# Performance work log

Measured on AMD Instinct MI355X. Metric: run time of the kernel, lower is better.

## Reference

```python
import jax, jax.numpy as jnp
import numpy as np

N_NODES = 100000
N_EDGES = 1600000
N_GRAPHS = 1000
HID = 64
NEG_SLOPE = 0.2


def _glorot(key, shape):
    fan_in, fan_out = shape[0], shape[-1]
    lim = float(np.sqrt(6.0 / (fan_in + fan_out)))
    return jax.random.uniform(key, shape, jnp.float32, -lim, lim)


def setup_inputs() -> dict:
    key = jax.random.key(0)
    ks = jax.random.split(key, 20)
    x = jax.random.normal(ks[0], (N_NODES, 1), jnp.float32)
    edge_index = jax.random.randint(ks[1], (2, N_EDGES), 0, N_NODES, jnp.int64)
    batch = jnp.sort(jax.random.randint(ks[2], (N_NODES,), 0, N_GRAPHS, jnp.int64))
    inp = {"x": x, "edge_index": edge_index, "batch": batch}
    # GATv2Conv layer 1 (in=3 -> out=HID, 1 head)
    inp["Wl1"] = _glorot(ks[3], (3, HID)); inp["bl1"] = jnp.zeros((HID,), jnp.float32)
    inp["Wr1"] = _glorot(ks[4], (3, HID)); inp["br1"] = jnp.zeros((HID,), jnp.float32)
    inp["a1"] = _glorot(ks[5], (HID, 1))[:, 0]; inp["b1"] = jnp.zeros((HID,), jnp.float32)
    # GATv2Conv layer 2 (HID -> HID)
    inp["Wl2"] = _glorot(ks[6], (HID, HID)); inp["bl2"] = jnp.zeros((HID,), jnp.float32)
    inp["Wr2"] = _glorot(ks[7], (HID, HID)); inp["br2"] = jnp.zeros((HID,), jnp.float32)
    inp["a2"] = _glorot(ks[8], (HID, 1))[:, 0]; inp["b2"] = jnp.zeros((HID,), jnp.float32)
    # lin2 (HID -> 2)
    inp["W3"] = _glorot(ks[9], (HID, 2)); inp["b3"] = jnp.zeros((2,), jnp.float32)
    return inp


def gatv2_layer(x, src, dst, Wl, bl, Wr, br, a, b):
    """GATv2Conv, 1 head, add_self_loops=True, negative_slope=0.2."""
    n = x.shape[0]
    xl = x @ Wl + bl  # source-side transform [N, C]
    xr = x @ Wr + br  # target-side transform [N, C]
    loops = jnp.arange(n, dtype=src.dtype)
    s = jnp.concatenate([src, loops])
    d = jnp.concatenate([dst, loops])
    # per-edge attention logit: a^T LeakyReLU(xl[j] + xr[i])
    e = jax.nn.leaky_relu(xl[s] + xr[d], NEG_SLOPE) @ a  # [E+N]
    # segment softmax over incoming edges of each dst node
    m = jax.ops.segment_max(e, d, num_segments=n)
    ex = jnp.exp(e - m[d])
    denom = jax.ops.segment_sum(ex, d, num_segments=n)
    alpha = ex / denom[d]
    out = jax.ops.segment_sum(alpha[:, None] * xl[s], d, num_segments=n)
    return out + b


def reference(x, edge_index, batch, Wl1, bl1, Wr1, br1, a1, b1,
              Wl2, bl2, Wr2, br2, a2, b2, W3, b3):
    n = x.shape[0]
    src, dst = edge_index[0], edge_index[1]
    ones = jnp.ones((src.shape[0],), jnp.float32)
    deg_in = jax.ops.segment_sum(ones, dst, num_segments=n)   # bincount(dst)
    deg_out = jax.ops.segment_sum(ones, src, num_segments=n)  # bincount(src)
    h = jnp.concatenate([x, deg_in[:, None], deg_out[:, None]], axis=1)  # [N,3]
    h = gatv2_layer(h, src, dst, Wl1, bl1, Wr1, br1, a1, b1)
    h = jnp.tanh(h)
    h = gatv2_layer(h, src, dst, Wl2, bl2, Wr2, br2, a2, b2)
    # global_max_pool over graphs
    g = jax.ops.segment_max(h, batch, num_segments=N_GRAPHS)  # [G, HID]
    return g @ W3 + b3  # [G, 2]
```

## Files before the change

kernel.cpp:

```cpp
#include <hip/hip_runtime.h>
#include <hip/hip_bf16.h>
#include <hip/hip_fp16.h>

#define HID 64
#define NEG_SLOPE 0.2f
#define BLK_E 8192
#define EDGE_CAP 6144
#define NDB 16

typedef _Float16 f16x2 __attribute__((ext_vector_type(2)));


__global__ void k_hist2(const int* __restrict__ src, const int* __restrict__ dst,
                        int* __restrict__ histS, int* __restrict__ histD,
                        int E, int NB, int NBLK) {
    __shared__ int hs[512], hd[512];
    int t = threadIdx.x, blk = blockIdx.x;
    for (int b = t; b < NB; b += 1024) { hs[b] = 0; hd[b] = 0; }
    __syncthreads();
    int base = blk * BLK_E;
    #pragma unroll
    for (int k = 0; k < BLK_E / 1024; ++k) {
        int i = base + k * 1024 + t;
        if (i < E) {
            atomicAdd(&hs[src[i] >> 8], 1);
            atomicAdd(&hd[dst[i] >> 8], 1);
        }
    }
    __syncthreads();
    for (int b = t; b < NB; b += 1024) {
        histS[b * NBLK + blk] = hs[b];
        histD[b * NBLK + blk] = hd[b];
    }
}

__global__ void k_binscan(int* __restrict__ histS, int* __restrict__ histD,
                          int* __restrict__ totS, int* __restrict__ totD,
                          int NB, int NBLK) {
    __shared__ int s[256];
    int b = blockIdx.x;
    int* hist = histS; int* tot = totS;
    if (b >= NB) { b -= NB; hist = histD; tot = totD; }
    int t = threadIdx.x;
    int v = (t < NBLK) ? hist[b * NBLK + t] : 0;
    s[t] = v;
    __syncthreads();
    for (int o = 1; o < 256; o <<= 1) {
        int u = (t >= o) ? s[t - o] : 0;
        __syncthreads();
        s[t] += u;
        __syncthreads();
    }
    if (t < NBLK) hist[b * NBLK + t] = s[t] - v;
    if (t == 255) tot[b] = s[255];
}

__global__ void k_binoffset(const int* __restrict__ totS, const int* __restrict__ totD,
                            int* __restrict__ bsS, int* __restrict__ bsD,
                            int NB, int E, int* __restrict__ row_off, int N) {
    __shared__ int s[512];
    int t = threadIdx.x;
    int v = (t < NB) ? totS[t] : 0;
    s[t] = v; __syncthreads();
    for (int o = 1; o < 512; o <<= 1) {
        int u = (t >= o) ? s[t - o] : 0;
        __syncthreads(); s[t] += u; __syncthreads();
    }
    if (t < NB) bsS[t] = s[t] - v;
    if (t == 0) bsS[NB] = E;
    __syncthreads();
    v = (t < NB) ? totD[t] : 0;
    s[t] = v; __syncthreads();
    for (int o = 1; o < 512; o <<= 1) {
        int u = (t >= o) ? s[t - o] : 0;
        __syncthreads(); s[t] += u; __syncthreads();
    }
    if (t < NB) bsD[t] = s[t] - v;
    if (t == 0) { bsD[NB] = E; row_off[N] = E; }
}

__global__ void k_scatter_bins(const int* __restrict__ src, const int* __restrict__ dst,
                               const int* __restrict__ histS, const int* __restrict__ histD,
                               const int* __restrict__ bsS, const int* __restrict__ bsD,
                               unsigned* __restrict__ packS, unsigned* __restrict__ packD,
                               int E, int NB, int NBLK) {
    __shared__ int baseS[512], baseD[512];
    int t = threadIdx.x, blk = blockIdx.x;
    for (int b = t; b < NB; b += 1024) {
        baseS[b] = bsS[b] + histS[b * NBLK + blk];
        baseD[b] = bsD[b] + histD[b * NBLK + blk];
    }
    __syncthreads();
    int base = blk * BLK_E;
    #pragma unroll
    for (int k = 0; k < BLK_E / 1024; ++k) {
        int i = base + k * 1024 + t;
        if (i < E) {
            int sv = src[i], dv = dst[i];
            int pD = atomicAdd(&baseD[dv >> 8], 1);
            packD[pD] = ((unsigned)(dv & 255) << 24) | (unsigned)sv;
            int pS = atomicAdd(&baseS[sv >> 8], 1);
            packS[pS] = (unsigned)(sv & 255);
        }
    }
}

__global__ void k_csr_bin(const unsigned* __restrict__ packD, const int* __restrict__ bsD,
                          int* __restrict__ row_off, float* __restrict__ deg_in,
                          int* __restrict__ csr_src, int N) {
    __shared__ int cnt[256], off[256], cur[256];
    __shared__ unsigned eb[EDGE_CAP];
    int b = blockIdx.x, t = threadIdx.x;
    int lo = bsD[b], hi = bsD[b + 1], ne = hi - lo;
    bool fits = (ne <= EDGE_CAP);
    if (t < 256) cnt[t] = 0;
    __syncthreads();
    for (int i = t; i < ne; i += 1024) {
        unsigned v = packD[lo + i];
        if (fits) eb[i] = v;
        atomicAdd(&cnt[v >> 24], 1);
    }
    __syncthreads();
    if (t < 256) off[t] = cnt[t];
    __syncthreads();
    for (int o = 1; o < 256; o <<= 1) {
        int u = 0;
        if (t < 256 && t >= o) u = off[t - o];
        __syncthreads();
        if (t < 256) off[t] += u;
        __syncthreads();
    }
    if (t < 256) {
        int ex = off[t] - cnt[t];
        cur[t] = lo + ex;
        int node = b * 256 + t;
        if (node < N) {
            row_off[node] = lo + ex;
            deg_in[node] = (float)cnt[t];
        }
    }
    __syncthreads();
    for (int i = t; i < ne; i += 1024) {
        unsigned v = fits ? eb[i] : packD[lo + i];
        int pos = atomicAdd(&cur[v >> 24], 1);
        csr_src[pos] = (int)(v & 0xFFFFFFu);
    }
}

__global__ void k_cnt_bin(const unsigned* __restrict__ packS, const int* __restrict__ bsS,
                          float* __restrict__ deg_out, int N) {
    __shared__ int cnt[256];
    int b = blockIdx.x, t = threadIdx.x;
    int lo = bsS[b], hi = bsS[b + 1];
    if (t < 256) cnt[t] = 0;
    __syncthreads();
    for (int i = lo + t; i < hi; i += 1024) atomicAdd(&cnt[packS[i] & 255], 1);
    __syncthreads();
    if (t < 256) {
        int node = b * 256 + t;
        if (node < N) deg_out[node] = (float)cnt[t];
    }
}


__global__ void k_deghist(const float* __restrict__ deg_in, int* __restrict__ dhist, int N) {
    __shared__ int h[64];
    int t = threadIdx.x, b = blockIdx.x;
    if (t < 64) h[t] = 0;
    __syncthreads();
    int chunk = (N + NDB - 1) / NDB;
    int lo = b * chunk, hi = lo + chunk; if (hi > N) hi = N;
    for (int i = lo + t; i < hi; i += 1024) {
        int dg = (int)deg_in[i]; if (dg > 63) dg = 63;
        atomicAdd(&h[dg], 1);
    }
    __syncthreads();
    if (t < 64) dhist[t * NDB + b] = h[t];
}

__global__ void k_degscan(int* __restrict__ dhist) {
    __shared__ int s[1024];
    int t = threadIdx.x;
    int v = dhist[t];
    s[t] = v; __syncthreads();
    for (int o = 1; o < 1024; o <<= 1) {
        int u = (t >= o) ? s[t - o] : 0;
        __syncthreads(); s[t] += u; __syncthreads();
    }
    dhist[t] = s[t] - v;
}

__global__ void k_degscatter(const float* __restrict__ deg_in, const int* __restrict__ dhist,
                             int* __restrict__ perm, int N) {
    __shared__ int cur[64];
    int t = threadIdx.x, b = blockIdx.x;
    if (t < 64) cur[t] = dhist[t * NDB + b];
    __syncthreads();
    int chunk = (N + NDB - 1) / NDB;
    int lo = b * chunk, hi = lo + chunk; if (hi > N) hi = N;
    for (int i = lo + t; i < hi; i += 1024) {
        int dg = (int)deg_in[i]; if (dg > 63) dg = 63;
        int p = atomicAdd(&cur[dg], 1);
        perm[p] = i;
    }
}


__global__ void k_xfrm1(const float* __restrict__ x, const float* __restrict__ deg_in,
                        const float* __restrict__ deg_out,
                        const float* __restrict__ Wl, const float* __restrict__ bl,
                        const float* __restrict__ Wr, const float* __restrict__ br,
                        __half* __restrict__ A, __half* __restrict__ B, int N) {
    int idx = blockIdx.x * blockDim.x + threadIdx.x;
    if (idx >= N * HID) return;
    int n = idx >> 6, c = idx & 63;
    float h0 = x[n], h1 = deg_in[n], h2 = deg_out[n];
    A[idx] = __float2half(h0 * Wl[c] + h1 * Wl[HID + c] + h2 * Wl[2 * HID + c] + bl[c]);
    B[idx] = __float2half(h0 * Wr[c] + h1 * Wr[HID + c] + h2 * Wr[2 * HID + c] + br[c]);
}

struct H8 { f16x2 h[8]; };

__device__ __forceinline__ f16x2 bch2(unsigned u) {
    return __builtin_bit_cast(f16x2, u);
}

__device__ __forceinline__ H8 ldrow(const uint4* __restrict__ T, size_t base) {
    uint4 r0 = T[base], r1 = T[base + 1];
    H8 o;
    o.h[0] = bch2(r0.x); o.h[1] = bch2(r0.y); o.h[2] = bch2(r0.z); o.h[3] = bch2(r0.w);
    o.h[4] = bch2(r1.x); o.h[5] = bch2(r1.y); o.h[6] = bch2(r1.z); o.h[7] = bch2(r1.w);
    return o;
}

__device__ __forceinline__ float logit16(const H8& a, const H8& x,
                                         const float* __restrict__ awf, f16x2 ns2) {
    float t = 0.0f;
    #pragma unroll
    for (int j = 0; j < 8; ++j) {
        f16x2 s = a.h[j] + x.h[j];
        f16x2 l = __builtin_elementwise_max(s, ns2 * s);
        t = fmaf((float)l.x, awf[2 * j], t);
        t = fmaf((float)l.y, awf[2 * j + 1], t);
    }
    return t;
}

__device__ __forceinline__ void accum16(float* __restrict__ acc, const H8& a, float w) {
    #pragma unroll
    for (int j = 0; j < 8; ++j) {
        acc[2 * j]     = fmaf((float)a.h[j].x, w, acc[2 * j]);
        acc[2 * j + 1] = fmaf((float)a.h[j].y, w, acc[2 * j + 1]);
    }
}

template <bool TANH>
__global__ void k_gat_fused(const int* __restrict__ csr_src, const int* __restrict__ row_off,
                            const int* __restrict__ perm,
                            const __half* __restrict__ Ah, const __half* __restrict__ Bh,
                            const float* __restrict__ aw, const float* __restrict__ bias,
                            float* __restrict__ out, int N) {
    int tid = blockIdx.x * blockDim.x + threadIdx.x;
    int r = tid >> 2;
    int gl = threadIdx.x & 3;
    if (r >= N) return;
    int d = perm[N - 1 - r];

    const uint4* A16 = (const uint4*)Ah;
    const uint4* B16 = (const uint4*)Bh;
    f16x2 ns2;
    ns2.x = (_Float16)NEG_SLOPE; ns2.y = (_Float16)NEG_SLOPE;

    float awf[16];
    {
        const float4* a4 = (const float4*)aw;
        #pragma unroll
        for (int j = 0; j < 4; ++j) {
            float4 v = a4[gl * 4 + j];
            awf[4 * j] = v.x; awf[4 * j + 1] = v.y; awf[4 * j + 2] = v.z; awf[4 * j + 3] = v.w;
        }
    }

    size_t rowbase = (size_t)d * 8 + gl * 2;
    H8 xh = ldrow(B16, rowbase);
    H8 as = ldrow(A16, rowbase);

    float t = logit16(as, xh, awf, ns2);
    t += __shfl_xor(t, 1); t += __shfl_xor(t, 2);
    float m = t, denom = 1.0f;
    float acc[16];
    #pragma unroll
    for (int j = 0; j < 8; ++j) {
        acc[2 * j] = (float)as.h[j].x;
        acc[2 * j + 1] = (float)as.h[j].y;
    }

    int lo = row_off[d], hi = row_off[d + 1];
    int k = lo;
    for (; k + 3 < hi; k += 4) {
        int s0 = csr_src[k], s1 = csr_src[k + 1], s2 = csr_src[k + 2], s3 = csr_src[k + 3];
        H8 a0 = ldrow(A16, (size_t)s0 * 8 + gl * 2);
        H8 a1 = ldrow(A16, (size_t)s1 * 8 + gl * 2);
        H8 a2 = ldrow(A16, (size_t)s2 * 8 + gl * 2);
        H8 a3 = ldrow(A16, (size_t)s3 * 8 + gl * 2);
        float t0 = logit16(a0, xh, awf, ns2);
        float t1 = logit16(a1, xh, awf, ns2);
        float t2 = logit16(a2, xh, awf, ns2);
        float t3 = logit16(a3, xh, awf, ns2);
        t0 += __shfl_xor(t0, 1); t1 += __shfl_xor(t1, 1);
        t2 += __shfl_xor(t2, 1); t3 += __shfl_xor(t3, 1);
        t0 += __shfl_xor(t0, 2); t1 += __shfl_xor(t1, 2);
        t2 += __shfl_xor(t2, 2); t3 += __shfl_xor(t3, 2);
        float mx = fmaxf(fmaxf(t0, t1), fmaxf(t2, t3));
        if (mx > m) {
            float sc = __expf(m - mx);
            denom *= sc;
            #pragma unroll
            for (int j = 0; j < 16; ++j) acc[j] *= sc;
            m = mx;
        }
        float w0 = __expf(t0 - m), w1 = __expf(t1 - m);
        float w2 = __expf(t2 - m), w3 = __expf(t3 - m);
        denom += (w0 + w1) + (w2 + w3);
        accum16(acc, a0, w0);
        accum16(acc, a1, w1);
        accum16(acc, a2, w2);
        accum16(acc, a3, w3);
    }
    for (; k < hi; ++k) {
        int s0 = csr_src[k];
        H8 a0 = ldrow(A16, (size_t)s0 * 8 + gl * 2);
        float t0 = logit16(a0, xh, awf, ns2);
        t0 += __shfl_xor(t0, 1); t0 += __shfl_xor(t0, 2);
        if (t0 > m) {
            float sc = __expf(m - t0);
            denom *= sc;
            #pragma unroll
            for (int j = 0; j < 16; ++j) acc[j] *= sc;
            m = t0;
        }
        float w0 = __expf(t0 - m);
        denom += w0;
        accum16(acc, a0, w0);
    }

    float inv = 1.0f / denom;
    const float4* b4 = (const float4*)bias;
    float4* o4 = (float4*)out;
    #pragma unroll
    for (int j = 0; j < 4; ++j) {
        float4 bv = b4[gl * 4 + j];
        float4 o;
        o.x = acc[4 * j] * inv + bv.x;
        o.y = acc[4 * j + 1] * inv + bv.y;
        o.z = acc[4 * j + 2] * inv + bv.z;
        o.w = acc[4 * j + 3] * inv + bv.w;
        if (TANH) { o.x = tanhf(o.x); o.y = tanhf(o.y); o.z = tanhf(o.z); o.w = tanhf(o.w); }
        o4[(size_t)d * 16 + gl * 4 + j] = o;
    }
}

__global__ __launch_bounds__(512) void k_xfrm2(
        const float* __restrict__ H,
        const float* __restrict__ Wl, const float* __restrict__ bl,
        const float* __restrict__ Wr, const float* __restrict__ br,
        __half* __restrict__ A, __half* __restrict__ B, int N) {
    __shared__ float wls[4096];
    __shared__ float wrs[4096];
    __shared__ float hst[64 * 66];
    int t = threadIdx.x;
    int base = blockIdx.x * 64;

    ((float4*)wls)[t * 2]     = ((const float4*)Wl)[t * 2];
    ((float4*)wls)[t * 2 + 1] = ((const float4*)Wl)[t * 2 + 1];
    ((float4*)wrs)[t * 2]     = ((const float4*)Wr)[t * 2];
    ((float4*)wrs)[t * 2 + 1] = ((const float4*)Wr)[t * 2 + 1];

    #pragma unroll
    for (int u = 0; u < 2; ++u) {
        int j = t * 2 + u;
        int nd = j >> 4, c4 = j & 15;
        int node = base + nd;
        float4 hv = (node < N) ? ((const float4*)H)[(size_t)node * 16 + c4]
                               : make_float4(0.f, 0.f, 0.f, 0.f);
        hst[(c4 * 4 + 0) * 66 + nd] = hv.x;
        hst[(c4 * 4 + 1) * 66 + nd] = hv.y;
        hst[(c4 * 4 + 2) * 66 + nd] = hv.z;
        hst[(c4 * 4 + 3) * 66 + nd] = hv.w;
    }
    __syncthreads();

    int w = t >> 6, l = t & 63;
    float acL[8] = {0, 0, 0, 0, 0, 0, 0, 0};
    float acR[8] = {0, 0, 0, 0, 0, 0, 0, 0};
    #pragma unroll 4
    for (int kk = 0; kk < 64; ++kk) {
        float hv = hst[kk * 66 + l];
        const float4* wl4 = (const float4*)&wls[kk * 64 + w * 8];
        const float4* wr4 = (const float4*)&wrs[kk * 64 + w * 8];
        float4 w0 = wl4[0], w1 = wl4[1];
        float4 r0 = wr4[0], r1 = wr4[1];
        acL[0] = fmaf(hv, w0.x, acL[0]); acL[1] = fmaf(hv, w0.y, acL[1]);
        acL[2] = fmaf(hv, w0.z, acL[2]); acL[3] = fmaf(hv, w0.w, acL[3]);
        acL[4] = fmaf(hv, w1.x, acL[4]); acL[5] = fmaf(hv, w1.y, acL[5]);
        acL[6] = fmaf(hv, w1.z, acL[6]); acL[7] = fmaf(hv, w1.w, acL[7]);
        acR[0] = fmaf(hv, r0.x, acR[0]); acR[1] = fmaf(hv, r0.y, acR[1]);
        acR[2] = fmaf(hv, r0.z, acR[2]); acR[3] = fmaf(hv, r0.w, acR[3]);
        acR[4] = fmaf(hv, r1.x, acR[4]); acR[5] = fmaf(hv, r1.y, acR[5]);
        acR[6] = fmaf(hv, r1.z, acR[6]); acR[7] = fmaf(hv, r1.w, acR[7]);
    }

    int node = base + l;
    if (node < N) {
        float4 bl0 = ((const float4*)bl)[w * 2], bl1 = ((const float4*)bl)[w * 2 + 1];
        float4 br0 = ((const float4*)br)[w * 2], br1 = ((const float4*)br)[w * 2 + 1];
        __half2* A2 = (__half2*)A;
        __half2* B2 = (__half2*)B;
        size_t bo = (size_t)node * 32 + w * 4;
        A2[bo + 0] = __floats2half2_rn(acL[0] + bl0.x, acL[1] + bl0.y);
        A2[bo + 1] = __floats2half2_rn(acL[2] + bl0.z, acL[3] + bl0.w);
        A2[bo + 2] = __floats2half2_rn(acL[4] + bl1.x, acL[5] + bl1.y);
        A2[bo + 3] = __floats2half2_rn(acL[6] + bl1.z, acL[7] + bl1.w);
        B2[bo + 0] = __floats2half2_rn(acR[0] + br0.x, acR[1] + br0.y);
        B2[bo + 1] = __floats2half2_rn(acR[2] + br0.z, acR[3] + br0.w);
        B2[bo + 2] = __floats2half2_rn(acR[4] + br1.x, acR[5] + br1.y);
        B2[bo + 3] = __floats2half2_rn(acR[6] + br1.z, acR[7] + br1.w);
    }
}

__global__ void k_gbounds(const int* __restrict__ batch, int* __restrict__ gstart,
                          int* __restrict__ gend, int N) {
    int i = blockIdx.x * blockDim.x + threadIdx.x;
    if (i >= N) return;
    int g = batch[i];
    if (i == 0 || batch[i - 1] != g) gstart[g] = i;
    if (i == N - 1 || batch[i + 1] != g) gend[g] = i + 1;
}

__global__ void k_pool_seg(const float* __restrict__ C, const float* __restrict__ b2,
                           const int* __restrict__ gstart, const int* __restrict__ gend,
                           float* __restrict__ gout, int G) {
    int w = (int)((blockIdx.x * (size_t)blockDim.x + threadIdx.x) >> 6);
    int lane = threadIdx.x & 63;
    if (w >= G) return;
    float acc = -INFINITY;
    int lo = gstart[w], hi = gend[w];
    for (int i = lo; i < hi; ++i) acc = fmaxf(acc, C[(size_t)i * HID + lane]);
    gout[(size_t)w * HID + lane] = acc + b2[lane];
}

__global__ void k_final(const float* __restrict__ gout, const float* __restrict__ W3,
                        const float* __restrict__ b3, float* __restrict__ out, int G) {
    int idx = blockIdx.x * blockDim.x + threadIdx.x;
    if (idx >= G * 2) return;
    int gi = idx >> 1, j = idx & 1;
    float sum = b3[j];
    #pragma unroll 8
    for (int kk = 0; kk < HID; ++kk) sum += gout[(size_t)gi * HID + kk] * W3[kk * 2 + j];
    out[idx] = sum;
}

extern "C" void kernel_launch(void* const* d_in, const int* in_sizes, int n_in,
                              void* d_out, int out_size, void* d_ws, size_t ws_size,
                              hipStream_t stream) {
    const float* x     = (const float*)d_in[0];
    const int*   ei    = (const int*)d_in[1];
    const int*   batch = (const int*)d_in[2];
    const float* Wl1 = (const float*)d_in[3];
    const float* bl1 = (const float*)d_in[4];
    const float* Wr1 = (const float*)d_in[5];
    const float* br1 = (const float*)d_in[6];
    const float* a1  = (const float*)d_in[7];
    const float* b1  = (const float*)d_in[8];
    const float* Wl2 = (const float*)d_in[9];
    const float* bl2 = (const float*)d_in[10];
    const float* Wr2 = (const float*)d_in[11];
    const float* br2 = (const float*)d_in[12];
    const float* a2  = (const float*)d_in[13];
    const float* b2  = (const float*)d_in[14];
    const float* W3  = (const float*)d_in[15];
    const float* b3  = (const float*)d_in[16];

    const int N = in_sizes[0];
    const int E = in_sizes[1] / 2;
    const int G = out_size / 2;
    const int NB = (N + 255) >> 8;
    const int NBLK = (E + BLK_E - 1) / BLK_E;

    float* ws = (float*)d_ws;
    size_t off = 0;
    float*  C  = ws + off; off += (size_t)N * HID;
    __half* Ah = (__half*)(ws + off); off += (size_t)N * HID / 2;
    __half* Bh = (__half*)(ws + off); off += (size_t)N * HID / 2;
    int*   row_off = (int*)(ws + off); off += N + 1;
    int*   csr_src = (int*)(ws + off); off += E;
    float* deg_in  = ws + off; off += N;
    float* deg_out = ws + off; off += N;
    int*   perm    = (int*)(ws + off); off += N;
    int*   dhist   = (int*)(ws + off); off += 1024;
    int*   bsS  = (int*)(ws + off); off += NB + 1;
    int*   bsD  = (int*)(ws + off); off += NB + 1;
    int*   totS = (int*)(ws + off); off += NB;
    int*   totD = (int*)(ws + off); off += NB;
    int*   gstart = (int*)(ws + off); off += G;
    int*   gend   = (int*)(ws + off); off += G;
    float* gout   = ws + off; off += (size_t)G * HID;

    unsigned* packD = (unsigned*)C;
    unsigned* packS = packD + E;
    int* histS = (int*)(packS + E);
    int* histD = histS + (size_t)NB * NBLK;

    const int* src  = ei;
    const int* dstp = ei + E;

    const int BT = 256;
    dim3 blk(BT);
    int grid_nodeC = (N * HID + BT - 1) / BT;
    int grid_g4    = (int)(((size_t)N * 4 + BT - 1) / BT);
    int grid_x2    = (N + 63) / 64;

    k_hist2<<<NBLK, 1024, 0, stream>>>(src, dstp, histS, histD, E, NB, NBLK);
    k_binscan<<<2 * NB, 256, 0, stream>>>(histS, histD, totS, totD, NB, NBLK);
    k_binoffset<<<1, 512, 0, stream>>>(totS, totD, bsS, bsD, NB, E, row_off, N);
    k_scatter_bins<<<NBLK, 1024, 0, stream>>>(src, dstp, histS, histD, bsS, bsD,
                                              packS, packD, E, NB, NBLK);
    k_csr_bin<<<NB, 1024, 0, stream>>>(packD, bsD, row_off, deg_in, csr_src, N);
    k_cnt_bin<<<NB, 1024, 0, stream>>>(packS, bsS, deg_out, N);

    k_deghist<<<NDB, 1024, 0, stream>>>(deg_in, dhist, N);
    k_degscan<<<1, 1024, 0, stream>>>(dhist);
    k_degscatter<<<NDB, 1024, 0, stream>>>(deg_in, dhist, perm, N);

    (void)hipMemsetAsync(gstart, 0, 2 * (size_t)G * sizeof(int), stream);
    k_gbounds<<<(N + BT - 1) / BT, blk, 0, stream>>>(batch, gstart, gend, N);

    k_xfrm1<<<grid_nodeC, blk, 0, stream>>>(x, deg_in, deg_out, Wl1, bl1, Wr1, br1, Ah, Bh, N);
    k_gat_fused<true><<<grid_g4, blk, 0, stream>>>(csr_src, row_off, perm, Ah, Bh, a1, b1, C, N);

    k_xfrm2<<<grid_x2, 512, 0, stream>>>(C, Wl2, bl2, Wr2, br2, Ah, Bh, N);
    k_gat_fused<false><<<grid_g4, blk, 0, stream>>>(csr_src, row_off, perm, Ah, Bh, a2, b2, C, N);

    k_pool_seg<<<(G * 64 + BT - 1) / BT, blk, 0, stream>>>(C, b2, gstart, gend, gout, G);
    k_final<<<(G * 2 + BT - 1) / BT, blk, 0, stream>>>(gout, W3, b3, (float*)d_out, G);
}
```

Baseline: 242.2 us.

## Software-pipeline GAT neighbor gathers and fuse pooling with final linear layer

The GAT aggregation loop now prefetches the next group of four source rows while it computes logits and accumulates the current group. Tail edges are handled by clamping indices and masking their logits, which replaces the scalar remainder loop. Graph bounds are found by binary search on the sorted batch array inside a single fused pool+linear kernel, removing the memset, the bounds kernel and the separate final kernel. The prefetch costs extra registers and some redundant loads on low-degree nodes, and the binary searches add reads of the batch array in every pooling wave.

```diff
diff --git a/kernel.cpp b/kernel.cpp
--- a/kernel.cpp
+++ b/kernel.cpp
@@ -296,52 +296,60 @@
     }
 
     int lo = row_off[d], hi = row_off[d + 1];
-    int k = lo;
-    for (; k + 3 < hi; k += 4) {
-        int s0 = csr_src[k], s1 = csr_src[k + 1], s2 = csr_src[k + 2], s3 = csr_src[k + 3];
-        H8 a0 = ldrow(A16, (size_t)s0 * 8 + gl * 2);
-        H8 a1 = ldrow(A16, (size_t)s1 * 8 + gl * 2);
-        H8 a2 = ldrow(A16, (size_t)s2 * 8 + gl * 2);
-        H8 a3 = ldrow(A16, (size_t)s3 * 8 + gl * 2);
-        float t0 = logit16(a0, xh, awf, ns2);
-        float t1 = logit16(a1, xh, awf, ns2);
-        float t2 = logit16(a2, xh, awf, ns2);
-        float t3 = logit16(a3, xh, awf, ns2);
-        t0 += __shfl_xor(t0, 1); t1 += __shfl_xor(t1, 1);
-        t2 += __shfl_xor(t2, 1); t3 += __shfl_xor(t3, 1);
-        t0 += __shfl_xor(t0, 2); t1 += __shfl_xor(t1, 2);
-        t2 += __shfl_xor(t2, 2); t3 += __shfl_xor(t3, 2);
-        float mx = fmaxf(fmaxf(t0, t1), fmaxf(t2, t3));
-        if (mx > m) {
-            float sc = __expf(m - mx);
-            denom *= sc;
-            #pragma unroll
-            for (int j = 0; j < 16; ++j) acc[j] *= sc;
-            m = mx;
+    if (lo < hi) {
+        int k = lo;
+        int ka = k + 1 < hi ? k + 1 : hi - 1;
+        int kb = k + 2 < hi ? k + 2 : hi - 1;
+        int kc = k + 3 < hi ? k + 3 : hi - 1;
+        int s0 = csr_src[k], s1 = csr_src[ka], s2 = csr_src[kb], s3 = csr_src[kc];
+        H8 c0 = ldrow(A16, (size_t)s0 * 8 + gl * 2);
+        H8 c1 = ldrow(A16, (size_t)s1 * 8 + gl * 2);
+        H8 c2 = ldrow(A16, (size_t)s2 * 8 + gl * 2);
+        H8 c3 = ldrow(A16, (size_t)s3 * 8 + gl * 2);
+        while (true) {
+            int kn = k + 4;
+            bool more = kn < hi;
+            H8 n0, n1, n2, n3;
+            if (more) {
+                int ja = kn + 1 < hi ? kn + 1 : hi - 1;
+                int jb = kn + 2 < hi ? kn + 2 : hi - 1;
+                int jc = kn + 3 < hi ? kn + 3 : hi - 1;
+                int u0 = csr_src[kn], u1 = csr_src[ja], u2 = csr_src[jb], u3 = csr_src[jc];
+                n0 = ldrow(A16, (size_t)u0 * 8 + gl * 2);
+                n1 = ldrow(A16, (size_t)u1 * 8 + gl * 2);
+                n2 = ldrow(A16, (size_t)u2 * 8 + gl * 2);
+                n3 = ldrow(A16, (size_t)u3 * 8 + gl * 2);
+            }
+            float t0 = logit16(c0, xh, awf, ns2);
+            float t1 = logit16(c1, xh, awf, ns2);
+            float t2 = logit16(c2, xh, awf, ns2);
+            float t3 = logit16(c3, xh, awf, ns2);
+            t0 += __shfl_xor(t0, 1); t1 += __shfl_xor(t1, 1);
+            t2 += __shfl_xor(t2, 1); t3 += __shfl_xor(t3, 1);
+            t0 += __shfl_xor(t0, 2); t1 += __shfl_xor(t1, 2);
+            t2 += __shfl_xor(t2, 2); t3 += __shfl_xor(t3, 2);
+            if (k + 1 >= hi) t1 = -1e30f;
+            if (k + 2 >= hi) t2 = -1e30f;
+            if (k + 3 >= hi) t3 = -1e30f;
+            float mx = fmaxf(fmaxf(t0, t1), fmaxf(t2, t3));
+            if (mx > m) {
+                float sc = __expf(m - mx);
+                denom *= sc;
+                #pragma unroll
+                for (int j = 0; j < 16; ++j) acc[j] *= sc;
+                m = mx;
+            }
+            float w0 = __expf(t0 - m), w1 = __expf(t1 - m);
+            float w2 = __expf(t2 - m), w3 = __expf(t3 - m);
+            denom += (w0 + w1) + (w2 + w3);
+            accum16(acc, c0, w0);
+            accum16(acc, c1, w1);
+            accum16(acc, c2, w2);
+            accum16(acc, c3, w3);
+            if (!more) break;
+            c0 = n0; c1 = n1; c2 = n2; c3 = n3;
+            k = kn;
         }
-        float w0 = __expf(t0 - m), w1 = __expf(t1 - m);
-        float w2 = __expf(t2 - m), w3 = __expf(t3 - m);
-        denom += (w0 + w1) + (w2 + w3);
-        accum16(acc, a0, w0);
-        accum16(acc, a1, w1);
-        accum16(acc, a2, w2);
-        accum16(acc, a3, w3);
-    }
-    for (; k < hi; ++k) {
-        int s0 = csr_src[k];
-        H8 a0 = ldrow(A16, (size_t)s0 * 8 + gl * 2);
-        float t0 = logit16(a0, xh, awf, ns2);
-        t0 += __shfl_xor(t0, 1); t0 += __shfl_xor(t0, 2);
-        if (t0 > m) {
-            float sc = __expf(m - t0);
-            denom *= sc;
-            #pragma unroll
-            for (int j = 0; j < 16; ++j) acc[j] *= sc;
-            m = t0;
-        }
-        float w0 = __expf(t0 - m);
-        denom += w0;
-        accum16(acc, a0, w0);
     }
 
     float inv = 1.0f / denom;
@@ -428,36 +436,40 @@
     }
 }
 
-__global__ void k_gbounds(const int* __restrict__ batch, int* __restrict__ gstart,
-                          int* __restrict__ gend, int N) {
-    int i = blockIdx.x * blockDim.x + threadIdx.x;
-    if (i >= N) return;
-    int g = batch[i];
-    if (i == 0 || batch[i - 1] != g) gstart[g] = i;
-    if (i == N - 1 || batch[i + 1] != g) gend[g] = i + 1;
-}
-
-__global__ void k_pool_seg(const float* __restrict__ C, const float* __restrict__ b2,
-                           const int* __restrict__ gstart, const int* __restrict__ gend,
-                           float* __restrict__ gout, int G) {
+__global__ void k_pool_final(const float* __restrict__ C, const float* __restrict__ b2,
+                             const int* __restrict__ batch,
+                             const float* __restrict__ W3, const float* __restrict__ b3,
+                             float* __restrict__ out, int N, int G) {
     int w = (int)((blockIdx.x * (size_t)blockDim.x + threadIdx.x) >> 6);
     int lane = threadIdx.x & 63;
     if (w >= G) return;
+    int lo = 0, hi = N;
+    while (lo < hi) { int mid = (lo + hi) >> 1; if (batch[mid] < w) lo = mid + 1; else hi = mid; }
+    int s0 = lo;
+    hi = N;
+    while (lo < hi) { int mid = (lo + hi) >> 1; if (batch[mid] < w + 1) lo = mid + 1; else hi = mid; }
+    int e0 = lo;
+
     float acc = -INFINITY;
-    int lo = gstart[w], hi = gend[w];
-    for (int i = lo; i < hi; ++i) acc = fmaxf(acc, C[(size_t)i * HID + lane]);
-    gout[(size_t)w * HID + lane] = acc + b2[lane];
-}
-
-__global__ void k_final(const float* __restrict__ gout, const float* __restrict__ W3,
-                        const float* __restrict__ b3, float* __restrict__ out, int G) {
-    int idx = blockIdx.x * blockDim.x + threadIdx.x;
-    if (idx >= G * 2) return;
-    int gi = idx >> 1, j = idx & 1;
-    float sum = b3[j];
-    #pragma unroll 8
-    for (int kk = 0; kk < HID; ++kk) sum += gout[(size_t)gi * HID + kk] * W3[kk * 2 + j];
-    out[idx] = sum;
+    int i = s0;
+    for (; i + 3 < e0; i += 4) {
+        float v0 = C[(size_t)i * HID + lane];
+        float v1 = C[(size_t)(i + 1) * HID + lane];
+        float v2 = C[(size_t)(i + 2) * HID + lane];
+        float v3 = C[(size_t)(i + 3) * HID + lane];
+        acc = fmaxf(acc, fmaxf(fmaxf(v0, v1), fmaxf(v2, v3)));
+    }
+    for (; i < e0; ++i) acc = fmaxf(acc, C[(size_t)i * HID + lane]);
+    float v = acc + b2[lane];
+
+    float p0 = v * W3[lane * 2];
+    float p1 = v * W3[lane * 2 + 1];
+    #pragma unroll
+    for (int o = 32; o; o >>= 1) { p0 += __shfl_xor(p0, o); p1 += __shfl_xor(p1, o); }
+    if (lane == 0) {
+        out[(size_t)w * 2]     = p0 + b3[0];
+        out[(size_t)w * 2 + 1] = p1 + b3[1];
+    }
 }
 
 extern "C" void kernel_launch(void* const* d_in, const int* in_sizes, int n_in,
@@ -502,9 +514,6 @@
     int*   bsD  = (int*)(ws + off); off += NB + 1;
     int*   totS = (int*)(ws + off); off += NB;
     int*   totD = (int*)(ws + off); off += NB;
-    int*   gstart = (int*)(ws + off); off += G;
-    int*   gend   = (int*)(ws + off); off += G;
-    float* gout   = ws + off; off += (size_t)G * HID;
 
     unsigned* packD = (unsigned*)C;
     unsigned* packS = packD + E;
@@ -532,15 +541,12 @@
     k_degscan<<<1, 1024, 0, stream>>>(dhist);
     k_degscatter<<<NDB, 1024, 0, stream>>>(deg_in, dhist, perm, N);
 
-    (void)hipMemsetAsync(gstart, 0, 2 * (size_t)G * sizeof(int), stream);
-    k_gbounds<<<(N + BT - 1) / BT, blk, 0, stream>>>(batch, gstart, gend, N);
-
     k_xfrm1<<<grid_nodeC, blk, 0, stream>>>(x, deg_in, deg_out, Wl1, bl1, Wr1, br1, Ah, Bh, N);
     k_gat_fused<true><<<grid_g4, blk, 0, stream>>>(csr_src, row_off, perm, Ah, Bh, a1, b1, C, N);
 
     k_xfrm2<<<grid_x2, 512, 0, stream>>>(C, Wl2, bl2, Wr2, br2, Ah, Bh, N);
     k_gat_fused<false><<<grid_g4, blk, 0, stream>>>(csr_src, row_off, perm, Ah, Bh, a2, b2, C, N);
 
-    k_pool_seg<<<(G * 64 + BT - 1) / BT, blk, 0, stream>>>(C, b2, gstart, gend, gout, G);
-    k_final<<<(G * 2 + BT - 1) / BT, blk, 0, stream>>>(gout, W3, b3, (float*)d_out, G);
-}
+    k_pool_final<<<(G * 64 + BT - 1) / BT, blk, 0, stream>>>(C, b2, batch, W3, b3,
+                                                             (float*)d_out, N, G);
+}
```

Measured after the change: 352.6 us. +45.6%, slower.
